# Kernel optimization log

Hardware: AMD Instinct MI355X
Metric: run time of the kernel (lower is better)

## Reference

```python
import jax, jax.numpy as jnp
import numpy as np

CAR_DIM = 8
ESC_MAX_AGENT = 32
HID = 256
ACTION_DIM = 30
NUM_STATES = 64
BATCH = 8192
ENC_OUT = 1 + CAR_DIM * ESC_MAX_AGENT          # 257
Q_IN = 1 + CAR_DIM + CAR_DIM * ESC_MAX_AGENT   # 265


def setup_inputs() -> dict:
    key = jax.random.key(0)
    ks = jax.random.split(key, 9)
    s = jax.random.normal(ks[0], (BATCH, CAR_DIM + NUM_STATES * CAR_DIM), dtype=jnp.float32)
    def lin(k, fan_in, fan_out):
        bound = 1.0 / np.sqrt(fan_in)
        kw, kb = jax.random.split(k)
        W = jax.random.uniform(kw, (fan_in, fan_out), jnp.float32, -bound, bound)
        b = jax.random.uniform(kb, (fan_out,), jnp.float32, -bound, bound)
        return W, b
    W1, b1 = lin(ks[1], CAR_DIM, HID)
    W2, b2 = lin(ks[2], HID, ENC_OUT)
    Qw1, Qb1 = lin(ks[3], Q_IN, HID)
    Qw2, Qb2 = lin(ks[4], HID, ACTION_DIM)
    return {"s": s, "W1": W1, "b1": b1, "W2": W2, "b2": b2,
            "Qw1": Qw1, "Qb1": Qb1, "Qw2": Qw2, "Qb2": Qb2}


def reference(s, W1, b1, W2, b2, Qw1, Qb1, Qw2, Qb2):
    B = s.shape[0]
    self_states = s[:, :CAR_DIM]                                   # [B, C]
    surr = s[:, CAR_DIM:].reshape(B, -1, CAR_DIM)                  # [B, N, C]
    # sentinel agents: any coordinate exactly == -1 is skipped
    valid = ~jnp.any(surr == -1.0, axis=-1)                        # [B, N] bool
    h = jax.nn.relu(jnp.einsum('bnc,ch->bnh', surr, W1) + b1)      # [B, N, HID]
    enc = jax.nn.relu(jnp.einsum('bnh,he->bne', h, W2) + b2)       # [B, N, ENC_OUT]
    sum_outputs = jnp.sum(enc * valid[:, :, None].astype(enc.dtype), axis=1)  # [B, ENC_OUT]
    x = jnp.concatenate([self_states, sum_outputs], axis=1)        # [B, Q_IN]
    q = jax.nn.relu(x @ Qw1 + Qb1) @ Qw2 + Qb2                     # [B, ACTION_DIM]
    return q
```

## Files before the change

kernel.cpp:

```cpp
#include <hip/hip_runtime.h>

#define CAR 8
#define SROW 520
#define HID 256
#define EOUT 257
#define XPAD 288
#define ADIM 30

typedef __attribute__((ext_vector_type(8))) short sh8;
typedef __attribute__((ext_vector_type(4))) float f32x4;

__device__ __forceinline__ short f2bf(float f) {
  unsigned u = __builtin_bit_cast(unsigned, f);
  u += 0x7fffu + ((u >> 16) & 1u);
  return (short)(u >> 16);
}
__device__ __forceinline__ unsigned f2bf2(float a, float b) {
  unsigned ua = __builtin_bit_cast(unsigned, a);
  ua += 0x7fffu + ((ua >> 16) & 1u);
  unsigned ub = __builtin_bit_cast(unsigned, b);
  ub += 0x7fffu + ((ub >> 16) & 1u);
  return __builtin_amdgcn_perm(ub, ua, 0x07060302);
}
__device__ __forceinline__ unsigned pkt(float a, float b) {
  return __builtin_amdgcn_perm(__builtin_bit_cast(unsigned, b),
                               __builtin_bit_cast(unsigned, a), 0x07060302);
}

__global__ void k_prep(const float* __restrict__ W1, const float* __restrict__ b1,
                       const float* __restrict__ W2,
                       const float* __restrict__ Qw1, const float* __restrict__ Qw2,
                       short* __restrict__ w1f, short* __restrict__ w2f,
                       short* __restrict__ w3f, short* __restrict__ wq2f) {
  int idx = blockIdx.x * 256 + threadIdx.x;
  if (idx < 8192) {
    int mt = idx >> 9, r = idx & 511, lane = r >> 3, j = r & 7;
    int quad = lane >> 4, m = lane & 15;
    int hid = mt * 16 + m;
    float v = (quad == 0) ? W1[j * HID + hid]
            : (quad == 1 && j == 0) ? b1[hid] : 0.0f;
    w1f[idx] = f2bf(v);
    return;
  }
  int i2 = idx - 8192;
  if (i2 < 69632) {
    int ks = i2 / 8704, r = i2 % 8704;
    int nt = r >> 9, r2 = r & 511, lane = r2 >> 3, j = r2 & 7;
    int quad = lane >> 4, m = lane & 15;
    int k = ks * 32 + quad * 8 + j, n = nt * 16 + m;
    float v = (n < EOUT) ? W2[k * EOUT + n] : 0.0f;
    w2f[i2] = f2bf(v);
    return;
  }
  int i3 = i2 - 69632;
  if (i3 < 73728) {
    int ks = i3 >> 13, r = i3 & 8191;
    int nt = r >> 9, r2 = r & 511, lane = r2 >> 3, j = r2 & 7;
    int quad = lane >> 4, m = lane & 15;
    int k = ks * 32 + quad * 8 + j, n = nt * 16 + m;
    float v = (k < 265) ? Qw1[k * HID + n] : 0.0f;
    w3f[i3] = f2bf(v);
    return;
  }
  int i4 = i3 - 73728;
  if (i4 < 8192) {
    int ks = i4 >> 10, r = i4 & 1023;
    int nt = r >> 9, r2 = r & 511, lane = r2 >> 3, j = r2 & 7;
    int quad = lane >> 4, m = lane & 15;
    int k = ks * 32 + quad * 8 + j, n = nt * 16 + m;
    float v = (n < ADIM) ? Qw2[k * ADIM + n] : 0.0f;
    wq2f[i4] = f2bf(v);
  }
}

__global__ __launch_bounds__(512, 4)
void k_enc(const float* __restrict__ s, const short* __restrict__ w1f,
           const short* __restrict__ w2f, const float* __restrict__ b2,
           float* __restrict__ so288, int B) {
  __shared__ __align__(16) short hlds[2][16384];
  __shared__ float ninvp[8];
  __shared__ float t16[8][16];

  const int tid = threadIdx.x;
  const int w = tid >> 6, lane = tid & 63;
  const int q = lane >> 4, m = lane & 15;
  const int we = w >> 2, g = w & 3;
  const size_t bg0 = 2 * (size_t)blockIdx.x;
  size_t bg = bg0 + we; if (bg >= (size_t)B) bg = B - 1;

  const float* srow0 = s + bg * SROW + CAR;
  int4 pk = {0, 0, 0, 0};
  bool inv = false;
  if (lane < 16) {
    const float* sr = srow0 + (g * 16 + lane) * CAR;
    float4 f0 = ((const float4*)sr)[0], f1 = ((const float4*)sr)[1];
    inv = (f0.x == -1.f) | (f0.y == -1.f) | (f0.z == -1.f) | (f0.w == -1.f) |
          (f1.x == -1.f) | (f1.y == -1.f) | (f1.z == -1.f) | (f1.w == -1.f);
    if (!inv) {
      pk.x = (int)f2bf2(f0.x, f0.y); pk.y = (int)f2bf2(f0.z, f0.w);
      pk.z = (int)f2bf2(f1.x, f1.y); pk.w = (int)f2bf2(f1.z, f1.w);
    }
  }
  const float vflag = inv ? 0.f : 1.f;
  unsigned long long bal = __ballot(inv);
  if (lane == 0) ninvp[w] = (float)__popcll(bal);

  if (w == 1 || w == 2) {
    size_t rr = bg0 + (w - 1); if (rr >= (size_t)B) rr = B - 1;
    if (lane < CAR)       so288[rr * XPAD + lane] = s[rr * SROW + lane];
    else if (lane < 16)   so288[rr * XPAD + 280 + (lane - 8)] = 0.f;
  }

  int4 p0;
  p0.x = __shfl(pk.x, m, 64); p0.y = __shfl(pk.y, m, 64);
  p0.z = __shfl(pk.z, m, 64); p0.w = __shfl(pk.w, m, 64);
  const float vv0 = __shfl(vflag, m, 64);
  if (q == 1) {
    p0.x = (vv0 != 0.f) ? 0x3f80 : 0; p0.y = p0.z = p0.w = 0;
  } else if (q >= 2) {
    p0.x = p0.y = p0.z = p0.w = 0;
  }
  sh8 bs = __builtin_bit_cast(sh8, p0);

#pragma unroll 4
  for (int mt = 0; mt < 16; ++mt) {
    sh8 af = *(const sh8*)(w1f + (mt * 64 + lane) * 8);
    f32x4 z = {0.f, 0.f, 0.f, 0.f};
    f32x4 c0 = __builtin_amdgcn_mfma_f32_16x16x32_bf16(af, bs, z, 0, 0, 0);
    const int hidb = mt * 16 + q * 4;
    const int ks = hidb >> 5, qB = (hidb >> 3) & 3, js = hidb & 7;
    uint2 k0;
    k0.x = pkt(fmaxf(c0[0], 0.f), fmaxf(c0[1], 0.f));
    k0.y = pkt(fmaxf(c0[2], 0.f), fmaxf(c0[3], 0.f));
    *(uint2*)(&hlds[we][((g * 8 + ks) * 64 + qB * 16 + m) * 8 + js]) = k0;
  }
  __syncthreads();

  f32x4 acc[4][2][2];
  f32x4 acc16 = {0.f, 0.f, 0.f, 0.f};
#pragma unroll
  for (int mtA = 0; mtA < 4; ++mtA)
#pragma unroll
    for (int i = 0; i < 2; ++i)
#pragma unroll
      for (int e = 0; e < 2; ++e) {
        f32x4 z = {0.f, 0.f, 0.f, 0.f};
        acc[mtA][i][e] = z;
      }
  const int t0 = 2 * w;
#pragma unroll
  for (int ks = 0; ks < 8; ++ks) {
    sh8 B0  = *(const sh8*)(w2f + ((ks * 17 + t0)     * 64 + lane) * 8);
    sh8 B1  = *(const sh8*)(w2f + ((ks * 17 + t0 + 1) * 64 + lane) * 8);
    sh8 B16 = *(const sh8*)(w2f + ((ks * 17 + 16)     * 64 + lane) * 8);
    sh8 A16 = *(const sh8*)(&hlds[we][((g * 8 + ks) * 64 + lane) * 8]);
    acc16 = __builtin_amdgcn_mfma_f32_16x16x32_bf16(A16, B16, acc16, 0, 0, 0);
#pragma unroll
    for (int e = 0; e < 2; ++e) {
      sh8 A0 = *(const sh8*)(&hlds[e][((0 * 8 + ks) * 64 + lane) * 8]);
      sh8 A1 = *(const sh8*)(&hlds[e][((1 * 8 + ks) * 64 + lane) * 8]);
      sh8 A2 = *(const sh8*)(&hlds[e][((2 * 8 + ks) * 64 + lane) * 8]);
      sh8 A3 = *(const sh8*)(&hlds[e][((3 * 8 + ks) * 64 + lane) * 8]);
      acc[0][0][e] = __builtin_amdgcn_mfma_f32_16x16x32_bf16(A0, B0, acc[0][0][e], 0, 0, 0);
      acc[1][0][e] = __builtin_amdgcn_mfma_f32_16x16x32_bf16(A1, B0, acc[1][0][e], 0, 0, 0);
      acc[2][0][e] = __builtin_amdgcn_mfma_f32_16x16x32_bf16(A2, B0, acc[2][0][e], 0, 0, 0);
      acc[3][0][e] = __builtin_amdgcn_mfma_f32_16x16x32_bf16(A3, B0, acc[3][0][e], 0, 0, 0);
      acc[0][1][e] = __builtin_amdgcn_mfma_f32_16x16x32_bf16(A0, B1, acc[0][1][e], 0, 0, 0);
      acc[1][1][e] = __builtin_amdgcn_mfma_f32_16x16x32_bf16(A1, B1, acc[1][1][e], 0, 0, 0);
      acc[2][1][e] = __builtin_amdgcn_mfma_f32_16x16x32_bf16(A2, B1, acc[2][1][e], 0, 0, 0);
      acc[3][1][e] = __builtin_amdgcn_mfma_f32_16x16x32_bf16(A3, B1, acc[3][1][e], 0, 0, 0);
    }
  }

  const float ninv[2] = {ninvp[0] + ninvp[1] + ninvp[2] + ninvp[3],
                         ninvp[4] + ninvp[5] + ninvp[6] + ninvp[7]};
#pragma unroll
  for (int i = 0; i < 2; ++i) {
    const int col = (t0 + i) * 16 + m;
    const float b2c = b2[col];
    const float rb2 = fmaxf(b2c, 0.f);
#pragma unroll
    for (int e = 0; e < 2; ++e) {
      float ssum = 0.f;
#pragma unroll
      for (int mtA = 0; mtA < 4; ++mtA)
#pragma unroll
        for (int r = 0; r < 4; ++r)
          ssum += fmaxf(acc[mtA][i][e][r] + b2c, 0.f);
      ssum += __shfl_xor(ssum, 16, 64);
      ssum += __shfl_xor(ssum, 32, 64);
      ssum -= ninv[e] * rb2;
      if (q == 0) {
        size_t rr = bg0 + e; if (rr >= (size_t)B) rr = B - 1;
        so288[rr * XPAD + CAR + col] = ssum;
      }
    }
  }
  {
    const int colc = 256 + m;
    const float b2c = (colc < EOUT) ? b2[colc] : 0.f;
    float s16 = 0.f;
#pragma unroll
    for (int r = 0; r < 4; ++r)
      s16 += fmaxf(acc16[r] + b2c, 0.f);
    s16 += __shfl_xor(s16, 16, 64);
    s16 += __shfl_xor(s16, 32, 64);
    if (q == 0) t16[w][m] = s16;
  }
  __syncthreads();
  if ((w == 0 || w == 4) && q == 0) {
    const int e = w >> 2;
    const int colc = 256 + m;
    const float b2c = (colc < EOUT) ? b2[colc] : 0.f;
    const float tot = t16[e * 4 + 0][m] + t16[e * 4 + 1][m] +
                      t16[e * 4 + 2][m] + t16[e * 4 + 3][m]
                    - ninv[e] * fmaxf(b2c, 0.f);
    size_t rr = bg0 + e; if (rr >= (size_t)B) rr = B - 1;
    so288[rr * XPAD + CAR + colc] = tot;
  }
}

__global__ __launch_bounds__(256, 2)
void k_q(const float* __restrict__ so288, const short* __restrict__ w3f,
         const float* __restrict__ Qb1, const short* __restrict__ wq2f,
         const float* __restrict__ Qb2, float* __restrict__ out, int B) {
  __shared__ __align__(16) short xf[2 * 9 * 64 * 8];
  __shared__ __align__(16) float H[32 * 260];
  const int tid = threadIdx.x;
  const int w = tid >> 6, lane = tid & 63;
  const int q = lane >> 4, m = lane & 15;
  const int b0 = blockIdx.x * 32;

#pragma unroll
  for (int it = 0; it < 5; ++it) {
    int sidx = tid + it * 256;
    if (sidx < 1152) {
      int mt = sidx / 576, rem = sidx % 576;
      int ks = rem >> 6, l = rem & 63;
      int lq = l >> 4, lm = l & 15;
      int row = b0 + mt * 16 + lm; if (row >= B) row = B - 1;
      const float* xp = so288 + (size_t)row * XPAD + ks * 32 + lq * 8;
      float4 xa = ((const float4*)xp)[0], xb = ((const float4*)xp)[1];
      int4 t = {(int)f2bf2(xa.x, xa.y), (int)f2bf2(xa.z, xa.w),
                (int)f2bf2(xb.x, xb.y), (int)f2bf2(xb.z, xb.w)};
      *(int4*)(xf + sidx * 8) = t;
    }
  }
  __syncthreads();

  f32x4 acc1[2][4];
#pragma unroll
  for (int mt = 0; mt < 2; ++mt)
#pragma unroll
    for (int i = 0; i < 4; ++i) {
      f32x4 z = {0.f, 0.f, 0.f, 0.f};
      acc1[mt][i] = z;
    }
#pragma unroll
  for (int ks = 0; ks < 9; ++ks) {
    sh8 A0 = *(const sh8*)(xf + ((0 * 9 + ks) * 64 + lane) * 8);
    sh8 A1 = *(const sh8*)(xf + ((1 * 9 + ks) * 64 + lane) * 8);
#pragma unroll
    for (int i = 0; i < 4; ++i) {
      sh8 Bf = *(const sh8*)(w3f + ((ks * 16 + 4 * w + i) * 64 + lane) * 8);
      acc1[0][i] = __builtin_amdgcn_mfma_f32_16x16x32_bf16(A0, Bf, acc1[0][i], 0, 0, 0);
      acc1[1][i] = __builtin_amdgcn_mfma_f32_16x16x32_bf16(A1, Bf, acc1[1][i], 0, 0, 0);
    }
  }
#pragma unroll
  for (int i = 0; i < 4; ++i) {
    const int hcol = (4 * w + i) * 16 + m;
    const float bq = Qb1[hcol];
#pragma unroll
    for (int mt = 0; mt < 2; ++mt)
#pragma unroll
      for (int r = 0; r < 4; ++r)
        H[(mt * 16 + q * 4 + r) * 260 + hcol] = fmaxf(acc1[mt][i][r] + bq, 0.f);
  }
  __syncthreads();

  const int mt2 = w >> 1, nt2 = w & 1;
  f32x4 acc2 = {0.f, 0.f, 0.f, 0.f};
#pragma unroll
  for (int ks = 0; ks < 8; ++ks) {
    const float* hp = H + (mt2 * 16 + m) * 260 + ks * 32 + q * 8;
    float4 ha = ((const float4*)hp)[0], hb = ((const float4*)hp)[1];
    int4 t = {(int)f2bf2(ha.x, ha.y), (int)f2bf2(ha.z, ha.w),
              (int)f2bf2(hb.x, hb.y), (int)f2bf2(hb.z, hb.w)};
    sh8 A2 = __builtin_bit_cast(sh8, t);
    sh8 Bf = *(const sh8*)(wq2f + ((ks * 2 + nt2) * 64 + lane) * 8);
    acc2 = __builtin_amdgcn_mfma_f32_16x16x32_bf16(A2, Bf, acc2, 0, 0, 0);
  }
  const int act = nt2 * 16 + m;
  if (act < ADIM) {
    const float bq = Qb2[act];
#pragma unroll
    for (int r = 0; r < 4; ++r) {
      const int row = b0 + mt2 * 16 + q * 4 + r;
      if (row < B) out[(size_t)row * ADIM + act] = acc2[r] + bq;
    }
  }
}

extern "C" void kernel_launch(void* const* d_in, const int* in_sizes, int n_in,
                              void* d_out, int out_size, void* d_ws, size_t ws_size,
                              hipStream_t stream) {
  const float* s   = (const float*)d_in[0];
  const float* W1  = (const float*)d_in[1];
  const float* b1  = (const float*)d_in[2];
  const float* W2  = (const float*)d_in[3];
  const float* b2  = (const float*)d_in[4];
  const float* Qw1 = (const float*)d_in[5];
  const float* Qb1 = (const float*)d_in[6];
  const float* Qw2 = (const float*)d_in[7];
  const float* Qb2 = (const float*)d_in[8];
  float* out = (float*)d_out;
  const int B = in_sizes[0] / SROW;

  char* wsb = (char*)d_ws;
  float* so288 = (float*)wsb;
  size_t off = (size_t)B * XPAD * sizeof(float);
  short* w1f  = (short*)(wsb + off);            off += 8192 * 2;
  short* w2f  = (short*)(wsb + off);            off += 69632 * 2;
  short* w3f  = (short*)(wsb + off);            off += 73728 * 2;
  short* wq2f = (short*)(wsb + off);

  const int prep_elems = 8192 + 69632 + 73728 + 8192;
  k_prep<<<(prep_elems + 255) / 256, 256, 0, stream>>>(W1, b1, W2, Qw1, Qw2,
                                                       w1f, w2f, w3f, wq2f);
  k_enc<<<(B + 1) / 2, 512, 0, stream>>>(s, w1f, w2f, b2, so288, B);
  k_q<<<(B + 31) / 32, 256, 0, stream>>>(so288, w3f, Qb1, wq2f, Qb2, out, B);
}
```

Baseline: 160.6 us.

## Switch encoder second GEMM to 32x32x16 MFMA with repacked weights and LDS layout

```diff
diff --git a/kernel.cpp b/kernel.cpp
--- a/kernel.cpp
+++ b/kernel.cpp
@@ -9,6 +9,7 @@
 
 typedef __attribute__((ext_vector_type(8))) short sh8;
 typedef __attribute__((ext_vector_type(4))) float f32x4;
+typedef __attribute__((ext_vector_type(16))) float f32x16;
 
 __device__ __forceinline__ short f2bf(float f) {
   unsigned u = __builtin_bit_cast(unsigned, f);
@@ -30,7 +31,8 @@
 __global__ void k_prep(const float* __restrict__ W1, const float* __restrict__ b1,
                        const float* __restrict__ W2,
                        const float* __restrict__ Qw1, const float* __restrict__ Qw2,
-                       short* __restrict__ w1f, short* __restrict__ w2f,
+                       short* __restrict__ w1f, short* __restrict__ w2f32,
+                       short* __restrict__ wt8,
                        short* __restrict__ w3f, short* __restrict__ wq2f) {
   int idx = blockIdx.x * 256 + threadIdx.x;
   if (idx < 8192) {
@@ -43,43 +45,50 @@
     return;
   }
   int i2 = idx - 8192;
-  if (i2 < 69632) {
-    int ks = i2 / 8704, r = i2 % 8704;
-    int nt = r >> 9, r2 = r & 511, lane = r2 >> 3, j = r2 & 7;
-    int quad = lane >> 4, m = lane & 15;
-    int k = ks * 32 + quad * 8 + j, n = nt * 16 + m;
-    float v = (n < EOUT) ? W2[k * EOUT + n] : 0.0f;
-    w2f[i2] = f2bf(v);
+  if (i2 < 65536) {
+    int ks = i2 >> 12, r = i2 & 4095;
+    int nt = r >> 9, r2 = r & 511, l = r2 >> 3, j = r2 & 7;
+    int k = ks * 16 + (l >> 5) * 8 + j;
+    int n = nt * 32 + (l & 31);
+    w2f32[i2] = f2bf(W2[k * EOUT + n]);
     return;
   }
-  int i3 = i2 - 69632;
-  if (i3 < 73728) {
-    int ks = i3 >> 13, r = i3 & 8191;
+  int i3 = i2 - 65536;
+  if (i3 < 4096) {
+    int ks32 = i3 >> 9, r2 = i3 & 511, l = r2 >> 3, j = r2 & 7;
+    int n = 256 + (l & 15);
+    int k = ks32 * 32 + ((l >> 4) & 3) * 8 + j;
+    wt8[i3] = (n < EOUT) ? f2bf(W2[k * EOUT + n]) : (short)0;
+    return;
+  }
+  int i4 = i3 - 4096;
+  if (i4 < 73728) {
+    int ks = i4 >> 13, r = i4 & 8191;
     int nt = r >> 9, r2 = r & 511, lane = r2 >> 3, j = r2 & 7;
     int quad = lane >> 4, m = lane & 15;
     int k = ks * 32 + quad * 8 + j, n = nt * 16 + m;
     float v = (k < 265) ? Qw1[k * HID + n] : 0.0f;
-    w3f[i3] = f2bf(v);
+    w3f[i4] = f2bf(v);
     return;
   }
-  int i4 = i3 - 73728;
-  if (i4 < 8192) {
-    int ks = i4 >> 10, r = i4 & 1023;
+  int i5 = i4 - 73728;
+  if (i5 < 8192) {
+    int ks = i5 >> 10, r = i5 & 1023;
     int nt = r >> 9, r2 = r & 511, lane = r2 >> 3, j = r2 & 7;
     int quad = lane >> 4, m = lane & 15;
     int k = ks * 32 + quad * 8 + j, n = nt * 16 + m;
     float v = (n < ADIM) ? Qw2[k * ADIM + n] : 0.0f;
-    wq2f[i4] = f2bf(v);
+    wq2f[i5] = f2bf(v);
   }
 }
 
 __global__ __launch_bounds__(512, 4)
 void k_enc(const float* __restrict__ s, const short* __restrict__ w1f,
-           const short* __restrict__ w2f, const float* __restrict__ b2,
-           float* __restrict__ so288, int B) {
-  __shared__ __align__(16) short hlds[2][16384];
+           const short* __restrict__ w2f32, const short* __restrict__ wt8,
+           const float* __restrict__ b2, float* __restrict__ so288, int B) {
+  __shared__ __align__(16) short hlds32[32768];
   __shared__ float ninvp[8];
-  __shared__ float t16[8][16];
+  __shared__ float red8[8];
 
   const int tid = threadIdx.x;
   const int w = tid >> 6, lane = tid & 63;
@@ -122,101 +131,98 @@
   }
   sh8 bs = __builtin_bit_cast(sh8, p0);
 
+  const int cI  = 2 * we + (g >> 1);
+  const int lpw = (g & 1) * 16 + m + 32 * (q >> 1);
+  const int j0  = (q & 1) * 4;
 #pragma unroll 4
   for (int mt = 0; mt < 16; ++mt) {
     sh8 af = *(const sh8*)(w1f + (mt * 64 + lane) * 8);
     f32x4 z = {0.f, 0.f, 0.f, 0.f};
     f32x4 c0 = __builtin_amdgcn_mfma_f32_16x16x32_bf16(af, bs, z, 0, 0, 0);
-    const int hidb = mt * 16 + q * 4;
-    const int ks = hidb >> 5, qB = (hidb >> 3) & 3, js = hidb & 7;
     uint2 k0;
     k0.x = pkt(fmaxf(c0[0], 0.f), fmaxf(c0[1], 0.f));
     k0.y = pkt(fmaxf(c0[2], 0.f), fmaxf(c0[3], 0.f));
-    *(uint2*)(&hlds[we][((g * 8 + ks) * 64 + qB * 16 + m) * 8 + js]) = k0;
+    *(uint2*)(&hlds32[((cI * 16 + mt) * 64 + lpw) * 8 + j0]) = k0;
   }
   __syncthreads();
 
-  f32x4 acc[4][2][2];
-  f32x4 acc16 = {0.f, 0.f, 0.f, 0.f};
-#pragma unroll
-  for (int mtA = 0; mtA < 4; ++mtA)
-#pragma unroll
-    for (int i = 0; i < 2; ++i)
-#pragma unroll
-      for (int e = 0; e < 2; ++e) {
-        f32x4 z = {0.f, 0.f, 0.f, 0.f};
-        acc[mtA][i][e] = z;
-      }
-  const int t0 = 2 * w;
-#pragma unroll
-  for (int ks = 0; ks < 8; ++ks) {
-    sh8 B0  = *(const sh8*)(w2f + ((ks * 17 + t0)     * 64 + lane) * 8);
-    sh8 B1  = *(const sh8*)(w2f + ((ks * 17 + t0 + 1) * 64 + lane) * 8);
-    sh8 B16 = *(const sh8*)(w2f + ((ks * 17 + 16)     * 64 + lane) * 8);
-    sh8 A16 = *(const sh8*)(&hlds[we][((g * 8 + ks) * 64 + lane) * 8]);
-    acc16 = __builtin_amdgcn_mfma_f32_16x16x32_bf16(A16, B16, acc16, 0, 0, 0);
-#pragma unroll
-    for (int e = 0; e < 2; ++e) {
-      sh8 A0 = *(const sh8*)(&hlds[e][((0 * 8 + ks) * 64 + lane) * 8]);
-      sh8 A1 = *(const sh8*)(&hlds[e][((1 * 8 + ks) * 64 + lane) * 8]);
-      sh8 A2 = *(const sh8*)(&hlds[e][((2 * 8 + ks) * 64 + lane) * 8]);
-      sh8 A3 = *(const sh8*)(&hlds[e][((3 * 8 + ks) * 64 + lane) * 8]);
-      acc[0][0][e] = __builtin_amdgcn_mfma_f32_16x16x32_bf16(A0, B0, acc[0][0][e], 0, 0, 0);
-      acc[1][0][e] = __builtin_amdgcn_mfma_f32_16x16x32_bf16(A1, B0, acc[1][0][e], 0, 0, 0);
-      acc[2][0][e] = __builtin_amdgcn_mfma_f32_16x16x32_bf16(A2, B0, acc[2][0][e], 0, 0, 0);
-      acc[3][0][e] = __builtin_amdgcn_mfma_f32_16x16x32_bf16(A3, B0, acc[3][0][e], 0, 0, 0);
-      acc[0][1][e] = __builtin_amdgcn_mfma_f32_16x16x32_bf16(A0, B1, acc[0][1][e], 0, 0, 0);
-      acc[1][1][e] = __builtin_amdgcn_mfma_f32_16x16x32_bf16(A1, B1, acc[1][1][e], 0, 0, 0);
-      acc[2][1][e] = __builtin_amdgcn_mfma_f32_16x16x32_bf16(A2, B1, acc[2][1][e], 0, 0, 0);
-      acc[3][1][e] = __builtin_amdgcn_mfma_f32_16x16x32_bf16(A3, B1, acc[3][1][e], 0, 0, 0);
-    }
-  }
-
-  const float ninv[2] = {ninvp[0] + ninvp[1] + ninvp[2] + ninvp[3],
-                         ninvp[4] + ninvp[5] + ninvp[6] + ninvp[7]};
-#pragma unroll
-  for (int i = 0; i < 2; ++i) {
-    const int col = (t0 + i) * 16 + m;
+  f32x16 z16;
+#pragma unroll
+  for (int r = 0; r < 16; ++r) z16[r] = 0.f;
+  f32x16 acc00 = z16, acc01 = z16, acc10 = z16, acc11 = z16;
+
+  const int c0i = 2 * we, c1i = 2 * we + 1;
+  const int nt0 = 2 * g, nt1 = 2 * g + 1;
+#pragma unroll
+  for (int ks = 0; ks < 16; ++ks) {
+    sh8 A0 = *(const sh8*)(&hlds32[((c0i * 16 + ks) * 64 + lane) * 8]);
+    sh8 A1 = *(const sh8*)(&hlds32[((c1i * 16 + ks) * 64 + lane) * 8]);
+    sh8 B0 = *(const sh8*)(w2f32 + ((ks * 8 + nt0) * 64 + lane) * 8);
+    sh8 B1 = *(const sh8*)(w2f32 + ((ks * 8 + nt1) * 64 + lane) * 8);
+    acc00 = __builtin_amdgcn_mfma_f32_32x32x16_bf16(A0, B0, acc00, 0, 0, 0);
+    acc10 = __builtin_amdgcn_mfma_f32_32x32x16_bf16(A1, B0, acc10, 0, 0, 0);
+    acc01 = __builtin_amdgcn_mfma_f32_32x32x16_bf16(A0, B1, acc01, 0, 0, 0);
+    acc11 = __builtin_amdgcn_mfma_f32_32x32x16_bf16(A1, B1, acc11, 0, 0, 0);
+  }
+
+  f32x4 acc8 = {0.f, 0.f, 0.f, 0.f};
+  const int c8  = 2 * we + (g >> 1);
+  const int lp8 = (g & 1) * 16 + (lane & 15) + 32 * ((lane >> 4) & 1);
+  const int kof = lane >> 5;
+#pragma unroll
+  for (int ks32 = 0; ks32 < 8; ++ks32) {
+    sh8 A8 = *(const sh8*)(&hlds32[((c8 * 16 + 2 * ks32 + kof) * 64 + lp8) * 8]);
+    sh8 B8 = *(const sh8*)(wt8 + (ks32 * 64 + lane) * 8);
+    acc8 = __builtin_amdgcn_mfma_f32_16x16x32_bf16(A8, B8, acc8, 0, 0, 0);
+  }
+
+  const float ninv_e = ninvp[4 * we] + ninvp[4 * we + 1] +
+                       ninvp[4 * we + 2] + ninvp[4 * we + 3];
+  size_t rr = bg0 + we; if (rr >= (size_t)B) rr = B - 1;
+  {
+    const int col = nt0 * 32 + (lane & 31);
     const float b2c = b2[col];
-    const float rb2 = fmaxf(b2c, 0.f);
-#pragma unroll
-    for (int e = 0; e < 2; ++e) {
-      float ssum = 0.f;
-#pragma unroll
-      for (int mtA = 0; mtA < 4; ++mtA)
-#pragma unroll
-        for (int r = 0; r < 4; ++r)
-          ssum += fmaxf(acc[mtA][i][e][r] + b2c, 0.f);
-      ssum += __shfl_xor(ssum, 16, 64);
-      ssum += __shfl_xor(ssum, 32, 64);
-      ssum -= ninv[e] * rb2;
-      if (q == 0) {
-        size_t rr = bg0 + e; if (rr >= (size_t)B) rr = B - 1;
-        so288[rr * XPAD + CAR + col] = ssum;
-      }
-    }
+    float ssum = 0.f;
+#pragma unroll
+    for (int r = 0; r < 16; ++r)
+      ssum += fmaxf(acc00[r] + b2c, 0.f) + fmaxf(acc10[r] + b2c, 0.f);
+    ssum += __shfl_xor(ssum, 32, 64);
+    ssum -= ninv_e * fmaxf(b2c, 0.f);
+    if (lane < 32) so288[rr * XPAD + CAR + col] = ssum;
   }
   {
-    const int colc = 256 + m;
-    const float b2c = (colc < EOUT) ? b2[colc] : 0.f;
-    float s16 = 0.f;
-#pragma unroll
-    for (int r = 0; r < 4; ++r)
-      s16 += fmaxf(acc16[r] + b2c, 0.f);
-    s16 += __shfl_xor(s16, 16, 64);
-    s16 += __shfl_xor(s16, 32, 64);
-    if (q == 0) t16[w][m] = s16;
+    const int col = nt1 * 32 + (lane & 31);
+    const float b2c = b2[col];
+    float ssum = 0.f;
+#pragma unroll
+    for (int r = 0; r < 16; ++r)
+      ssum += fmaxf(acc01[r] + b2c, 0.f) + fmaxf(acc11[r] + b2c, 0.f);
+    ssum += __shfl_xor(ssum, 32, 64);
+    ssum -= ninv_e * fmaxf(b2c, 0.f);
+    if (lane < 32) so288[rr * XPAD + CAR + col] = ssum;
+  }
+  {
+    const int n8 = lane & 15;
+    const float b8c = (n8 == 0) ? b2[256] : 0.f;
+    float s8 = 0.f;
+#pragma unroll
+    for (int r = 0; r < 4; ++r) s8 += fmaxf(acc8[r] + b8c, 0.f);
+    s8 += __shfl_xor(s8, 16, 64);
+    s8 += __shfl_xor(s8, 32, 64);
+    if (lane == 0) red8[w] = s8;
   }
   __syncthreads();
-  if ((w == 0 || w == 4) && q == 0) {
-    const int e = w >> 2;
-    const int colc = 256 + m;
-    const float b2c = (colc < EOUT) ? b2[colc] : 0.f;
-    const float tot = t16[e * 4 + 0][m] + t16[e * 4 + 1][m] +
-                      t16[e * 4 + 2][m] + t16[e * 4 + 3][m]
-                    - ninv[e] * fmaxf(b2c, 0.f);
-    size_t rr = bg0 + e; if (rr >= (size_t)B) rr = B - 1;
-    so288[rr * XPAD + CAR + colc] = tot;
+  if ((w == 0 || w == 4) && lane < 16) {
+    const int e2 = w >> 2;
+    size_t rr2 = bg0 + e2; if (rr2 >= (size_t)B) rr2 = B - 1;
+    float v = 0.f;
+    if (lane == 0) {
+      const float ninv2 = ninvp[4 * e2] + ninvp[4 * e2 + 1] +
+                          ninvp[4 * e2 + 2] + ninvp[4 * e2 + 3];
+      v = red8[4 * e2] + red8[4 * e2 + 1] + red8[4 * e2 + 2] + red8[4 * e2 + 3]
+        - ninv2 * fmaxf(b2[256], 0.f);
+    }
+    so288[rr2 * XPAD + CAR + 256 + lane] = v;
   }
 }
 
@@ -320,14 +326,15 @@
   char* wsb = (char*)d_ws;
   float* so288 = (float*)wsb;
   size_t off = (size_t)B * XPAD * sizeof(float);
-  short* w1f  = (short*)(wsb + off);            off += 8192 * 2;
-  short* w2f  = (short*)(wsb + off);            off += 69632 * 2;
-  short* w3f  = (short*)(wsb + off);            off += 73728 * 2;
-  short* wq2f = (short*)(wsb + off);
-
-  const int prep_elems = 8192 + 69632 + 73728 + 8192;
+  short* w1f   = (short*)(wsb + off);           off += 8192 * 2;
+  short* w2f32 = (short*)(wsb + off);           off += 65536 * 2;
+  short* wt8   = (short*)(wsb + off);           off += 4096 * 2;
+  short* w3f   = (short*)(wsb + off);           off += 73728 * 2;
+  short* wq2f  = (short*)(wsb + off);
+
+  const int prep_elems = 8192 + 65536 + 4096 + 73728 + 8192;
   k_prep<<<(prep_elems + 255) / 256, 256, 0, stream>>>(W1, b1, W2, Qw1, Qw2,
-                                                       w1f, w2f, w3f, wq2f);
-  k_enc<<<(B + 1) / 2, 512, 0, stream>>>(s, w1f, w2f, b2, so288, B);
+                                                       w1f, w2f32, wt8, w3f, wq2f);
+  k_enc<<<(B + 1) / 2, 512, 0, stream>>>(s, w1f, w2f32, wt8, b2, so288, B);
   k_q<<<(B + 31) / 32, 256, 0, stream>>>(so288, w3f, Qb1, wq2f, Qb2, out, B);
 }
```

Result: slower. 168.4 us (+4.9%).

## Fold b2 bias and validity mask into an extra K-slice of the encoder GEMM

Applied to the files above, without the earlier changes.

```diff
diff --git a/kernel.cpp b/kernel.cpp
--- a/kernel.cpp
+++ b/kernel.cpp
@@ -28,7 +28,7 @@
 }
 
 __global__ void k_prep(const float* __restrict__ W1, const float* __restrict__ b1,
-                       const float* __restrict__ W2,
+                       const float* __restrict__ W2, const float* __restrict__ b2,
                        const float* __restrict__ Qw1, const float* __restrict__ Qw2,
                        short* __restrict__ w1f, short* __restrict__ w2f,
                        short* __restrict__ w3f, short* __restrict__ wq2f) {
@@ -43,16 +43,20 @@
     return;
   }
   int i2 = idx - 8192;
-  if (i2 < 69632) {
+  if (i2 < 78336) {
     int ks = i2 / 8704, r = i2 % 8704;
     int nt = r >> 9, r2 = r & 511, lane = r2 >> 3, j = r2 & 7;
     int quad = lane >> 4, m = lane & 15;
     int k = ks * 32 + quad * 8 + j, n = nt * 16 + m;
-    float v = (n < EOUT) ? W2[k * EOUT + n] : 0.0f;
+    float v = 0.0f;
+    if (n < EOUT) {
+      if (k < 256)       v = W2[k * EOUT + n];
+      else if (k == 256) v = b2[n];
+    }
     w2f[i2] = f2bf(v);
     return;
   }
-  int i3 = i2 - 69632;
+  int i3 = i2 - 78336;
   if (i3 < 73728) {
     int ks = i3 >> 13, r = i3 & 8191;
     int nt = r >> 9, r2 = r & 511, lane = r2 >> 3, j = r2 & 7;
@@ -75,11 +79,9 @@
 
 __global__ __launch_bounds__(512, 4)
 void k_enc(const float* __restrict__ s, const short* __restrict__ w1f,
-           const short* __restrict__ w2f, const float* __restrict__ b2,
-           float* __restrict__ so288, int B) {
-  __shared__ __align__(16) short hlds[2][16384];
-  __shared__ float ninvp[8];
-  __shared__ float t16[8][16];
+           const short* __restrict__ w2f, float* __restrict__ so288, int B) {
+  __shared__ __align__(16) short hlds[36864];
+  __shared__ float red8[8];
 
   const int tid = threadIdx.x;
   const int w = tid >> 6, lane = tid & 63;
@@ -102,8 +104,6 @@
     }
   }
   const float vflag = inv ? 0.f : 1.f;
-  unsigned long long bal = __ballot(inv);
-  if (lane == 0) ninvp[w] = (float)__popcll(bal);
 
   if (w == 1 || w == 2) {
     size_t rr = bg0 + (w - 1); if (rr >= (size_t)B) rr = B - 1;
@@ -122,6 +122,7 @@
   }
   sh8 bs = __builtin_bit_cast(sh8, p0);
 
+  const int sbase = (we * 4 + g) * 9;
 #pragma unroll 4
   for (int mt = 0; mt < 16; ++mt) {
     sh8 af = *(const sh8*)(w1f + (mt * 64 + lane) * 8);
@@ -132,7 +133,11 @@
     uint2 k0;
     k0.x = pkt(fmaxf(c0[0], 0.f), fmaxf(c0[1], 0.f));
     k0.y = pkt(fmaxf(c0[2], 0.f), fmaxf(c0[3], 0.f));
-    *(uint2*)(&hlds[we][((g * 8 + ks) * 64 + qB * 16 + m) * 8 + js]) = k0;
+    *(uint2*)(&hlds[(sbase + ks) * 512 + (qB * 16 + m) * 8 + js]) = k0;
+  }
+  {
+    int4 ov = {(q == 0 && vv0 != 0.f) ? 0x3f80 : 0, 0, 0, 0};
+    *(int4*)(&hlds[(sbase + 8) * 512 + lane * 8]) = ov;
   }
   __syncthreads();
 
@@ -149,18 +154,16 @@
       }
   const int t0 = 2 * w;
 #pragma unroll
-  for (int ks = 0; ks < 8; ++ks) {
+  for (int ks = 0; ks < 9; ++ks) {
     sh8 B0  = *(const sh8*)(w2f + ((ks * 17 + t0)     * 64 + lane) * 8);
     sh8 B1  = *(const sh8*)(w2f + ((ks * 17 + t0 + 1) * 64 + lane) * 8);
     sh8 B16 = *(const sh8*)(w2f + ((ks * 17 + 16)     * 64 + lane) * 8);
-    sh8 A16 = *(const sh8*)(&hlds[we][((g * 8 + ks) * 64 + lane) * 8]);
-    acc16 = __builtin_amdgcn_mfma_f32_16x16x32_bf16(A16, B16, acc16, 0, 0, 0);
 #pragma unroll
     for (int e = 0; e < 2; ++e) {
-      sh8 A0 = *(const sh8*)(&hlds[e][((0 * 8 + ks) * 64 + lane) * 8]);
-      sh8 A1 = *(const sh8*)(&hlds[e][((1 * 8 + ks) * 64 + lane) * 8]);
-      sh8 A2 = *(const sh8*)(&hlds[e][((2 * 8 + ks) * 64 + lane) * 8]);
-      sh8 A3 = *(const sh8*)(&hlds[e][((3 * 8 + ks) * 64 + lane) * 8]);
+      sh8 A0 = *(const sh8*)(&hlds[((e * 4 + 0) * 9 + ks) * 512 + lane * 8]);
+      sh8 A1 = *(const sh8*)(&hlds[((e * 4 + 1) * 9 + ks) * 512 + lane * 8]);
+      sh8 A2 = *(const sh8*)(&hlds[((e * 4 + 2) * 9 + ks) * 512 + lane * 8]);
+      sh8 A3 = *(const sh8*)(&hlds[((e * 4 + 3) * 9 + ks) * 512 + lane * 8]);
       acc[0][0][e] = __builtin_amdgcn_mfma_f32_16x16x32_bf16(A0, B0, acc[0][0][e], 0, 0, 0);
       acc[1][0][e] = __builtin_amdgcn_mfma_f32_16x16x32_bf16(A1, B0, acc[1][0][e], 0, 0, 0);
       acc[2][0][e] = __builtin_amdgcn_mfma_f32_16x16x32_bf16(A2, B0, acc[2][0][e], 0, 0, 0);
@@ -169,16 +172,20 @@
       acc[1][1][e] = __builtin_amdgcn_mfma_f32_16x16x32_bf16(A1, B1, acc[1][1][e], 0, 0, 0);
       acc[2][1][e] = __builtin_amdgcn_mfma_f32_16x16x32_bf16(A2, B1, acc[2][1][e], 0, 0, 0);
       acc[3][1][e] = __builtin_amdgcn_mfma_f32_16x16x32_bf16(A3, B1, acc[3][1][e], 0, 0, 0);
-    }
-  }
-
-  const float ninv[2] = {ninvp[0] + ninvp[1] + ninvp[2] + ninvp[3],
-                         ninvp[4] + ninvp[5] + ninvp[6] + ninvp[7]};
+      if (we == e) {
+        if (g == 0)      acc16 = __builtin_amdgcn_mfma_f32_16x16x32_bf16(A0, B16, acc16, 0, 0, 0);
+        else if (g == 1) acc16 = __builtin_amdgcn_mfma_f32_16x16x32_bf16(A1, B16, acc16, 0, 0, 0);
+        else if (g == 2) acc16 = __builtin_amdgcn_mfma_f32_16x16x32_bf16(A2, B16, acc16, 0, 0, 0);
+        else             acc16 = __builtin_amdgcn_mfma_f32_16x16x32_bf16(A3, B16, acc16, 0, 0, 0);
+      }
+    }
+  }
+
+  size_t rr0 = bg0;     if (rr0 >= (size_t)B) rr0 = B - 1;
+  size_t rr1 = bg0 + 1; if (rr1 >= (size_t)B) rr1 = B - 1;
 #pragma unroll
   for (int i = 0; i < 2; ++i) {
     const int col = (t0 + i) * 16 + m;
-    const float b2c = b2[col];
-    const float rb2 = fmaxf(b2c, 0.f);
 #pragma unroll
     for (int e = 0; e < 2; ++e) {
       float ssum = 0.f;
@@ -186,37 +193,29 @@
       for (int mtA = 0; mtA < 4; ++mtA)
 #pragma unroll
         for (int r = 0; r < 4; ++r)
-          ssum += fmaxf(acc[mtA][i][e][r] + b2c, 0.f);
+          ssum += fmaxf(acc[mtA][i][e][r], 0.f);
       ssum += __shfl_xor(ssum, 16, 64);
       ssum += __shfl_xor(ssum, 32, 64);
-      ssum -= ninv[e] * rb2;
-      if (q == 0) {
-        size_t rr = bg0 + e; if (rr >= (size_t)B) rr = B - 1;
-        so288[rr * XPAD + CAR + col] = ssum;
-      }
+      if (q == 0)
+        so288[(e ? rr1 : rr0) * XPAD + CAR + col] = ssum;
     }
   }
   {
-    const int colc = 256 + m;
-    const float b2c = (colc < EOUT) ? b2[colc] : 0.f;
     float s16 = 0.f;
 #pragma unroll
-    for (int r = 0; r < 4; ++r)
-      s16 += fmaxf(acc16[r] + b2c, 0.f);
+    for (int r = 0; r < 4; ++r) s16 += fmaxf(acc16[r], 0.f);
     s16 += __shfl_xor(s16, 16, 64);
     s16 += __shfl_xor(s16, 32, 64);
-    if (q == 0) t16[w][m] = s16;
+    if (lane == 0) red8[w] = s16;
   }
   __syncthreads();
-  if ((w == 0 || w == 4) && q == 0) {
-    const int e = w >> 2;
-    const int colc = 256 + m;
-    const float b2c = (colc < EOUT) ? b2[colc] : 0.f;
-    const float tot = t16[e * 4 + 0][m] + t16[e * 4 + 1][m] +
-                      t16[e * 4 + 2][m] + t16[e * 4 + 3][m]
-                    - ninv[e] * fmaxf(b2c, 0.f);
-    size_t rr = bg0 + e; if (rr >= (size_t)B) rr = B - 1;
-    so288[rr * XPAD + CAR + colc] = tot;
+  if ((w == 0 || w == 4) && lane < 16) {
+    const int e2 = w >> 2;
+    size_t rr2 = bg0 + e2; if (rr2 >= (size_t)B) rr2 = B - 1;
+    float v = 0.f;
+    if (lane == 0)
+      v = red8[4 * e2] + red8[4 * e2 + 1] + red8[4 * e2 + 2] + red8[4 * e2 + 3];
+    so288[rr2 * XPAD + CAR + 256 + lane] = v;
   }
 }
 
@@ -321,13 +320,13 @@
   float* so288 = (float*)wsb;
   size_t off = (size_t)B * XPAD * sizeof(float);
   short* w1f  = (short*)(wsb + off);            off += 8192 * 2;
-  short* w2f  = (short*)(wsb + off);            off += 69632 * 2;
+  short* w2f  = (short*)(wsb + off);            off += 78336 * 2;
   short* w3f  = (short*)(wsb + off);            off += 73728 * 2;
   short* wq2f = (short*)(wsb + off);
 
-  const int prep_elems = 8192 + 69632 + 73728 + 8192;
-  k_prep<<<(prep_elems + 255) / 256, 256, 0, stream>>>(W1, b1, W2, Qw1, Qw2,
+  const int prep_elems = 8192 + 78336 + 73728 + 8192;
+  k_prep<<<(prep_elems + 255) / 256, 256, 0, stream>>>(W1, b1, W2, b2, Qw1, Qw2,
                                                        w1f, w2f, w3f, wq2f);
-  k_enc<<<(B + 1) / 2, 512, 0, stream>>>(s, w1f, w2f, b2, so288, B);
+  k_enc<<<(B + 1) / 2, 512, 0, stream>>>(s, w1f, w2f, so288, B);
   k_q<<<(B + 31) / 32, 256, 0, stream>>>(so288, w3f, Qb1, wq2f, Qb2, out, B);
 }
```

Result: slower. 167.6 us (+4.4%).

## Fold bias into MFMA accumulators, reuse A fragments, halve k_q row tile

Applied to the files above, without the earlier changes.

```diff
diff --git a/kernel.cpp b/kernel.cpp
--- a/kernel.cpp
+++ b/kernel.cpp
@@ -136,31 +136,33 @@
   }
   __syncthreads();
 
+  const int t0 = 2 * w;
+  const float bi0  = b2[t0 * 16 + m];
+  const float bi1  = b2[t0 * 16 + 16 + m];
+  const float bi16 = (m == 0) ? b2[256] : 0.f;
   f32x4 acc[4][2][2];
-  f32x4 acc16 = {0.f, 0.f, 0.f, 0.f};
+  f32x4 acc16 = {bi16, bi16, bi16, bi16};
 #pragma unroll
   for (int mtA = 0; mtA < 4; ++mtA)
 #pragma unroll
-    for (int i = 0; i < 2; ++i)
-#pragma unroll
-      for (int e = 0; e < 2; ++e) {
-        f32x4 z = {0.f, 0.f, 0.f, 0.f};
-        acc[mtA][i][e] = z;
-      }
-  const int t0 = 2 * w;
+    for (int e = 0; e < 2; ++e) {
+      f32x4 c0 = {bi0, bi0, bi0, bi0};
+      f32x4 c1 = {bi1, bi1, bi1, bi1};
+      acc[mtA][0][e] = c0;
+      acc[mtA][1][e] = c1;
+    }
 #pragma unroll
   for (int ks = 0; ks < 8; ++ks) {
     sh8 B0  = *(const sh8*)(w2f + ((ks * 17 + t0)     * 64 + lane) * 8);
     sh8 B1  = *(const sh8*)(w2f + ((ks * 17 + t0 + 1) * 64 + lane) * 8);
     sh8 B16 = *(const sh8*)(w2f + ((ks * 17 + 16)     * 64 + lane) * 8);
-    sh8 A16 = *(const sh8*)(&hlds[we][((g * 8 + ks) * 64 + lane) * 8]);
-    acc16 = __builtin_amdgcn_mfma_f32_16x16x32_bf16(A16, B16, acc16, 0, 0, 0);
 #pragma unroll
     for (int e = 0; e < 2; ++e) {
-      sh8 A0 = *(const sh8*)(&hlds[e][((0 * 8 + ks) * 64 + lane) * 8]);
-      sh8 A1 = *(const sh8*)(&hlds[e][((1 * 8 + ks) * 64 + lane) * 8]);
-      sh8 A2 = *(const sh8*)(&hlds[e][((2 * 8 + ks) * 64 + lane) * 8]);
-      sh8 A3 = *(const sh8*)(&hlds[e][((3 * 8 + ks) * 64 + lane) * 8]);
+      sh8 A0 = *(const sh8*)(&hlds[e][(0 * 8 + ks) * 512 + lane * 8]);
+      sh8 A1 = *(const sh8*)(&hlds[e][(1 * 8 + ks) * 512 + lane * 8]);
+      sh8 A2 = *(const sh8*)(&hlds[e][(2 * 8 + ks) * 512 + lane * 8]);
+      sh8 A3 = *(const sh8*)(&hlds[e][(3 * 8 + ks) * 512 + lane * 8]);
+      __builtin_amdgcn_s_setprio(1);
       acc[0][0][e] = __builtin_amdgcn_mfma_f32_16x16x32_bf16(A0, B0, acc[0][0][e], 0, 0, 0);
       acc[1][0][e] = __builtin_amdgcn_mfma_f32_16x16x32_bf16(A1, B0, acc[1][0][e], 0, 0, 0);
       acc[2][0][e] = __builtin_amdgcn_mfma_f32_16x16x32_bf16(A2, B0, acc[2][0][e], 0, 0, 0);
@@ -169,6 +171,13 @@
       acc[1][1][e] = __builtin_amdgcn_mfma_f32_16x16x32_bf16(A1, B1, acc[1][1][e], 0, 0, 0);
       acc[2][1][e] = __builtin_amdgcn_mfma_f32_16x16x32_bf16(A2, B1, acc[2][1][e], 0, 0, 0);
       acc[3][1][e] = __builtin_amdgcn_mfma_f32_16x16x32_bf16(A3, B1, acc[3][1][e], 0, 0, 0);
+      if (we == e) {
+        if (g == 0)      acc16 = __builtin_amdgcn_mfma_f32_16x16x32_bf16(A0, B16, acc16, 0, 0, 0);
+        else if (g == 1) acc16 = __builtin_amdgcn_mfma_f32_16x16x32_bf16(A1, B16, acc16, 0, 0, 0);
+        else if (g == 2) acc16 = __builtin_amdgcn_mfma_f32_16x16x32_bf16(A2, B16, acc16, 0, 0, 0);
+        else             acc16 = __builtin_amdgcn_mfma_f32_16x16x32_bf16(A3, B16, acc16, 0, 0, 0);
+      }
+      __builtin_amdgcn_s_setprio(0);
     }
   }
 
@@ -177,8 +186,8 @@
 #pragma unroll
   for (int i = 0; i < 2; ++i) {
     const int col = (t0 + i) * 16 + m;
-    const float b2c = b2[col];
-    const float rb2 = fmaxf(b2c, 0.f);
+    const float bic = (i == 0) ? bi0 : bi1;
+    const float rb2 = fmaxf(bic, 0.f);
 #pragma unroll
     for (int e = 0; e < 2; ++e) {
       float ssum = 0.f;
@@ -186,7 +195,7 @@
       for (int mtA = 0; mtA < 4; ++mtA)
 #pragma unroll
         for (int r = 0; r < 4; ++r)
-          ssum += fmaxf(acc[mtA][i][e][r] + b2c, 0.f);
+          ssum += fmaxf(acc[mtA][i][e][r], 0.f);
       ssum += __shfl_xor(ssum, 16, 64);
       ssum += __shfl_xor(ssum, 32, 64);
       ssum -= ninv[e] * rb2;
@@ -197,26 +206,23 @@
     }
   }
   {
-    const int colc = 256 + m;
-    const float b2c = (colc < EOUT) ? b2[colc] : 0.f;
     float s16 = 0.f;
 #pragma unroll
     for (int r = 0; r < 4; ++r)
-      s16 += fmaxf(acc16[r] + b2c, 0.f);
+      s16 += fmaxf(acc16[r], 0.f);
     s16 += __shfl_xor(s16, 16, 64);
     s16 += __shfl_xor(s16, 32, 64);
     if (q == 0) t16[w][m] = s16;
   }
   __syncthreads();
   if ((w == 0 || w == 4) && q == 0) {
-    const int e = w >> 2;
-    const int colc = 256 + m;
-    const float b2c = (colc < EOUT) ? b2[colc] : 0.f;
-    const float tot = t16[e * 4 + 0][m] + t16[e * 4 + 1][m] +
-                      t16[e * 4 + 2][m] + t16[e * 4 + 3][m]
-                    - ninv[e] * fmaxf(b2c, 0.f);
-    size_t rr = bg0 + e; if (rr >= (size_t)B) rr = B - 1;
-    so288[rr * XPAD + CAR + colc] = tot;
+    const int e2 = w >> 2;
+    const float b2c = (m == 0) ? b2[256] : 0.f;
+    const float tot = t16[e2 * 4 + 0][m] + t16[e2 * 4 + 1][m] +
+                      t16[e2 * 4 + 2][m] + t16[e2 * 4 + 3][m]
+                    - ninv[e2] * fmaxf(b2c, 0.f);
+    size_t rr2 = bg0 + e2; if (rr2 >= (size_t)B) rr2 = B - 1;
+    so288[rr2 * XPAD + CAR + 256 + m] = tot;
   }
 }
 
@@ -224,21 +230,20 @@
 void k_q(const float* __restrict__ so288, const short* __restrict__ w3f,
          const float* __restrict__ Qb1, const short* __restrict__ wq2f,
          const float* __restrict__ Qb2, float* __restrict__ out, int B) {
-  __shared__ __align__(16) short xf[2 * 9 * 64 * 8];
-  __shared__ __align__(16) float H[32 * 260];
+  __shared__ __align__(16) short xf[9 * 64 * 8];
+  __shared__ __align__(16) float H[16 * 260];
   const int tid = threadIdx.x;
   const int w = tid >> 6, lane = tid & 63;
   const int q = lane >> 4, m = lane & 15;
-  const int b0 = blockIdx.x * 32;
-
-#pragma unroll
-  for (int it = 0; it < 5; ++it) {
+  const int b0 = blockIdx.x * 16;
+
+#pragma unroll
+  for (int it = 0; it < 3; ++it) {
     int sidx = tid + it * 256;
-    if (sidx < 1152) {
-      int mt = sidx / 576, rem = sidx % 576;
-      int ks = rem >> 6, l = rem & 63;
+    if (sidx < 576) {
+      int ks = sidx >> 6, l = sidx & 63;
       int lq = l >> 4, lm = l & 15;
-      int row = b0 + mt * 16 + lm; if (row >= B) row = B - 1;
+      int row = b0 + lm; if (row >= B) row = B - 1;
       const float* xp = so288 + (size_t)row * XPAD + ks * 32 + lq * 8;
       float4 xa = ((const float4*)xp)[0], xb = ((const float4*)xp)[1];
       int4 t = {(int)f2bf2(xa.x, xa.y), (int)f2bf2(xa.z, xa.w),
@@ -248,23 +253,19 @@
   }
   __syncthreads();
 
-  f32x4 acc1[2][4];
-#pragma unroll
-  for (int mt = 0; mt < 2; ++mt)
-#pragma unroll
-    for (int i = 0; i < 4; ++i) {
-      f32x4 z = {0.f, 0.f, 0.f, 0.f};
-      acc1[mt][i] = z;
-    }
+  f32x4 acc1[4];
+#pragma unroll
+  for (int i = 0; i < 4; ++i) {
+    f32x4 z = {0.f, 0.f, 0.f, 0.f};
+    acc1[i] = z;
+  }
 #pragma unroll
   for (int ks = 0; ks < 9; ++ks) {
-    sh8 A0 = *(const sh8*)(xf + ((0 * 9 + ks) * 64 + lane) * 8);
-    sh8 A1 = *(const sh8*)(xf + ((1 * 9 + ks) * 64 + lane) * 8);
+    sh8 A0 = *(const sh8*)(xf + (ks * 64 + lane) * 8);
 #pragma unroll
     for (int i = 0; i < 4; ++i) {
       sh8 Bf = *(const sh8*)(w3f + ((ks * 16 + 4 * w + i) * 64 + lane) * 8);
-      acc1[0][i] = __builtin_amdgcn_mfma_f32_16x16x32_bf16(A0, Bf, acc1[0][i], 0, 0, 0);
-      acc1[1][i] = __builtin_amdgcn_mfma_f32_16x16x32_bf16(A1, Bf, acc1[1][i], 0, 0, 0);
+      acc1[i] = __builtin_amdgcn_mfma_f32_16x16x32_bf16(A0, Bf, acc1[i], 0, 0, 0);
     }
   }
 #pragma unroll
@@ -272,32 +273,31 @@
     const int hcol = (4 * w + i) * 16 + m;
     const float bq = Qb1[hcol];
 #pragma unroll
-    for (int mt = 0; mt < 2; ++mt)
-#pragma unroll
-      for (int r = 0; r < 4; ++r)
-        H[(mt * 16 + q * 4 + r) * 260 + hcol] = fmaxf(acc1[mt][i][r] + bq, 0.f);
+    for (int r = 0; r < 4; ++r)
+      H[(q * 4 + r) * 260 + hcol] = fmaxf(acc1[i][r] + bq, 0.f);
   }
   __syncthreads();
 
-  const int mt2 = w >> 1, nt2 = w & 1;
-  f32x4 acc2 = {0.f, 0.f, 0.f, 0.f};
-#pragma unroll
-  for (int ks = 0; ks < 8; ++ks) {
-    const float* hp = H + (mt2 * 16 + m) * 260 + ks * 32 + q * 8;
-    float4 ha = ((const float4*)hp)[0], hb = ((const float4*)hp)[1];
-    int4 t = {(int)f2bf2(ha.x, ha.y), (int)f2bf2(ha.z, ha.w),
-              (int)f2bf2(hb.x, hb.y), (int)f2bf2(hb.z, hb.w)};
-    sh8 A2 = __builtin_bit_cast(sh8, t);
-    sh8 Bf = *(const sh8*)(wq2f + ((ks * 2 + nt2) * 64 + lane) * 8);
-    acc2 = __builtin_amdgcn_mfma_f32_16x16x32_bf16(A2, Bf, acc2, 0, 0, 0);
-  }
-  const int act = nt2 * 16 + m;
-  if (act < ADIM) {
-    const float bq = Qb2[act];
-#pragma unroll
-    for (int r = 0; r < 4; ++r) {
-      const int row = b0 + mt2 * 16 + q * 4 + r;
-      if (row < B) out[(size_t)row * ADIM + act] = acc2[r] + bq;
+  if (w < 2) {
+    f32x4 acc2 = {0.f, 0.f, 0.f, 0.f};
+#pragma unroll
+    for (int ks = 0; ks < 8; ++ks) {
+      const float* hp = H + m * 260 + ks * 32 + q * 8;
+      float4 ha = ((const float4*)hp)[0], hb = ((const float4*)hp)[1];
+      int4 t = {(int)f2bf2(ha.x, ha.y), (int)f2bf2(ha.z, ha.w),
+                (int)f2bf2(hb.x, hb.y), (int)f2bf2(hb.z, hb.w)};
+      sh8 A2 = __builtin_bit_cast(sh8, t);
+      sh8 Bf = *(const sh8*)(wq2f + ((ks * 2 + w) * 64 + lane) * 8);
+      acc2 = __builtin_amdgcn_mfma_f32_16x16x32_bf16(A2, Bf, acc2, 0, 0, 0);
+    }
+    const int act = w * 16 + m;
+    if (act < ADIM) {
+      const float bq = Qb2[act];
+#pragma unroll
+      for (int r = 0; r < 4; ++r) {
+        const int row = b0 + q * 4 + r;
+        if (row < B) out[(size_t)row * ADIM + act] = acc2[r] + bq;
+      }
     }
   }
 }
@@ -329,5 +329,5 @@
   k_prep<<<(prep_elems + 255) / 256, 256, 0, stream>>>(W1, b1, W2, Qw1, Qw2,
                                                        w1f, w2f, w3f, wq2f);
   k_enc<<<(B + 1) / 2, 512, 0, stream>>>(s, w1f, w2f, b2, so288, B);
-  k_q<<<(B + 31) / 32, 256, 0, stream>>>(so288, w3f, Qb1, wq2f, Qb2, out, B);
-}
+  k_q<<<(B + 15) / 16, 256, 0, stream>>>(so288, w3f, Qb1, wq2f, Qb2, out, B);
+}
```

Result: no change. 162.7 us (+1.3%).
